# Kernel optimization log

Measured on AMD Instinct MI355X. Metric: run time of the kernel, lower is better.

The kernel has to match this reference:

```python
import jax, jax.numpy as jnp
import numpy as np

N = 10000      # atoms
F = 32         # nr_atom_basis
H = 7          # nr_heads
C = F * H      # nr_coefficients = 224
E = 200000     # edges
NRBF = 50
CUTOFF = 5.0
EPS = 1e-8


def _seg_sum(x, idx, n):
    return jax.ops.segment_sum(x, idx, num_segments=n)


def _seg_mean(x, idx, n):
    # torch scatter_reduce 'mean' with include_self=False: sum/count, 0 for empty segments
    s = _seg_sum(x, idx, n)
    cnt = _seg_sum(jnp.ones((x.shape[0],), x.dtype), idx, n)
    cnt = jnp.maximum(cnt, 1.0).reshape((n,) + (1,) * (x.ndim - 1))
    return s / cnt


def _scatter_softmax(w, idx, n):
    m = jax.ops.segment_max(w, idx, num_segments=n)
    m = jnp.where(jnp.isfinite(m), m, 0.0)  # guard empty segments
    e = jnp.exp(w - m[idx])
    s = _seg_sum(e, idx, n)
    return e / s[idx]


def setup_inputs():
    key = jax.random.key(0)
    ks = jax.random.split(key, 16)
    def w(k, shape, scale=0.1):
        return jax.random.normal(k, shape, jnp.float32) * scale
    return {
        "h": w(ks[0], (N, F), 1.0),
        "x": w(ks[1], (N, 3), 1.0),
        "v": w(ks[2], (N, 3), 0.1),
        "pairlist": jax.random.randint(ks[3], (2, E), 0, N),
        "w_in": w(ks[4], (2 * F, NRBF)), "b_in": jnp.zeros((NRBF,), jnp.float32),
        "w_e1": w(ks[5], (2 * F + NRBF + 1, F)), "b_e1": jnp.zeros((F,), jnp.float32),
        "w_e2": w(ks[6], (F, F)), "b_e2": jnp.zeros((F,), jnp.float32),
        "w_att": w(ks[7], (F, H)), "b_att": jnp.zeros((H,), jnp.float32),
        "w_n1": w(ks[8], (F + C + F, F)), "b_n1": jnp.zeros((F,), jnp.float32),
        "w_n2": w(ks[9], (F, F)), "b_n2": jnp.zeros((F,), jnp.float32),
        "w_pn1": w(ks[10], (C, F)), "b_pn1": jnp.zeros((F,), jnp.float32),
        "w_pn2": w(ks[11], (F, F)), "b_pn2": jnp.zeros((F,), jnp.float32),
        "w_v1": w(ks[12], (F, F)), "b_v1": jnp.zeros((F,), jnp.float32),
        "w_v2": w(ks[13], (F, 1)),
        "w_xmix": w(ks[14], (C, C)),
        "w_vmix": w(ks[15], (C, 1)),
    }


def reference(h, x, v, pairlist, w_in, b_in, w_e1, b_e1, w_e2, b_e2,
              w_att, b_att, w_n1, b_n1, w_n2, b_n2, w_pn1, b_pn1,
              w_pn2, b_pn2, w_v1, b_v1, w_v2, w_xmix, w_vmix):
    act = jax.nn.silu
    idx_i, idx_j = pairlist[0], pairlist[1]
    n = h.shape[0]

    r_ij = x[idx_j] - x[idx_i]                      # [E,3]
    d_ij = jnp.linalg.norm(r_ij, axis=-1)           # [E]
    dir_ij = r_ij / (d_ij[:, None] + EPS)           # [E,3]

    # edge model: continuous-filter conv with concatenation
    h_cat = jnp.concatenate([h[idx_i], h[idx_j]], axis=-1)           # [E,2F]
    centers = jnp.linspace(0.0, CUTOFF, NRBF)
    width = centers[1] - centers[0]
    rbf = jnp.exp(-0.5 * ((d_ij[:, None] - centers) / width) ** 2)   # [E,NRBF]
    filt = rbf * (h_cat @ w_in + b_in)                               # [E,NRBF]
    edge_in = jnp.concatenate([h_cat, filt, d_ij[:, None]], axis=-1)
    h_ij_edge = act(edge_in @ w_e1 + b_e1) @ w_e2 + b_e2             # [E,F]

    # semantic attention (scatter softmax over edges grouped by idx_i)
    att_w = jax.nn.celu(h_ij_edge @ w_att + b_att, alpha=2.0)        # [E,H]
    cut = 0.5 * (jnp.cos(jnp.pi * d_ij / CUTOFF) + 1.0) * (d_ij < CUTOFF)
    att = _scatter_softmax(att_w * cut[:, None], idx_i, n)           # [E,H]
    # einsum('pf,ph->pfh').reshape -> f-major, h-minor
    h_ij_sem = (h_ij_edge[:, :, None] * att[:, None, :]).reshape(-1, C)  # [E,C]
    h_i_sem = _seg_sum(h_ij_sem, idx_i, n)                           # [N,C]

    # equivariant combinations + spatial attention
    comb = jnp.tanh(h_ij_sem @ w_xmix)[:, :, None] * dir_ij[:, None, :]  # [E,C,3]
    comb_mean = _seg_mean(comb, idx_i, n)                            # [N,C,3]
    cnsq = jnp.sum(comb_mean ** 2, axis=-1)                          # [N,C]
    h_i_spatial = act(act(cnsq @ w_pn1 + b_pn1) @ w_pn2 + b_pn2)     # [N,F]

    # node update
    node_in = jnp.concatenate([h, h_i_sem, h_i_spatial], axis=-1)
    h_upd = h + act(act(node_in @ w_n1 + b_n1) @ w_n2 + b_n2)        # [N,F]

    # velocity update
    v_ij = jnp.einsum('ecx,c->ex', comb, w_vmix[:, 0])               # [E,3]
    dv = _seg_mean(v_ij, idx_i, n)                                   # [N,3]
    gate = 2.0 * jax.nn.sigmoid(act(h @ w_v1 + b_v1) @ w_v2)         # [N,1]
    v_upd = gate * v + dv
    x_upd = x + v_upd
    return h_upd, x_upd, v_upd
```

## Files before the change

kernel.cpp:

```cpp
#include <hip/hip_runtime.h>
#include <hip/hip_bf16.h>
#include <math.h>

typedef unsigned short u16;
typedef __attribute__((ext_vector_type(8))) short bf16x8;
typedef __attribute__((ext_vector_type(4))) float f32x4;

constexpr int kF    = 32;
constexpr int kH    = 7;
constexpr int kC    = 224;
constexpr int kRBF  = 50;
constexpr int kM    = 128;
constexpr int kStr  = 232;
constexpr int kUSt  = 36;
constexpr int kEM   = 128;
constexpr int kAStr = 136;
constexpr int kBStr = 40;
constexpr float kCut = 5.0f;
constexpr float kEps = 1e-8f;

__device__ __forceinline__ float silu_f(float a) { return a / (1.f + __expf(-a)); }
__device__ __forceinline__ float tanh_f(float x) {
    float e = __expf(2.f * x);
    return 1.f - 2.f / (e + 1.f);
}
__device__ __forceinline__ float bf2f(u16 u) {
    union { unsigned int i; float f; } v; v.i = ((unsigned int)u) << 16; return v.f;
}
__device__ __forceinline__ u16 f2bf(float f) {
    union { float f; unsigned int i; } v; v.f = f;
    unsigned int x = v.i;
    unsigned int round = ((x >> 16) & 1u) + 0x7fffu;
    return (u16)((x + round) >> 16);
}
__device__ __forceinline__ unsigned pk2(float a, float b) {
    union { __hip_bfloat162 h; unsigned u; } v;
    v.h = __float22bfloat162_rn(make_float2(a, b));
    return v.u;
}

__global__ __launch_bounds__(256) void init_kernel(
    const float* __restrict__ wx, const float* __restrict__ w_in,
    const float* __restrict__ w_e1, const float* __restrict__ w_e2,
    const float* __restrict__ w_att, const float* __restrict__ b_e2,
    const float* __restrict__ b_att, const float* __restrict__ w_n1,
    const int* __restrict__ pl,
    u16* __restrict__ wxT, u16* __restrict__ W1T, u16* __restrict__ W2T,
    u16* __restrict__ W3T, u16* __restrict__ W24T, u16* __restrict__ Wn1hT,
    float* __restrict__ b24, int* __restrict__ counts, int E_)
{
    int idx = blockIdx.x * 256 + threadIdx.x;
    if (idx < kC * kC) {
        int c = idx / kC, k = idx - c * kC;
        wxT[idx] = f2bf(wx[k * kC + c]);
    }
    for (int e = idx; e < E_; e += gridDim.x * 256) atomicAdd(&counts[pl[e]], 1);

    if (blockIdx.x == 0) {
        int t = threadIdx.x;
        for (int i = t; i < 64 * 64; i += 256) {
            int n = i >> 6, k = i & 63;
            W1T[i] = f2bf((n < kRBF) ? w_in[k * kRBF + n] : 0.f);
        }
        for (int i = t; i < 32 * 128; i += 256) {
            int n = i >> 7, k = i & 127;
            W2T[i] = f2bf((k < 115) ? w_e1[k * kF + n] : 0.f);
        }
        for (int i = t; i < 32 * 32; i += 256) {
            int n = i >> 5, k = i & 31;
            W3T[i] = f2bf(w_e2[k * kF + n]);
        }
        for (int i = t; i < 16 * 32; i += 256) {
            int n = i >> 5, k = i & 31;
            float a = 0.f;
            if (n < kH) for (int o = 0; o < kF; o++) a += w_e2[k * kF + o] * w_att[o * kH + n];
            W24T[i] = f2bf(a);
        }
        if (t < kH) {
            float a = b_att[t];
            for (int o = 0; o < kF; o++) a += b_e2[o] * w_att[o * kH + t];
            b24[t] = a;
        }
    }
    if (blockIdx.x == 1) {
        int t = threadIdx.x;
        for (int i = t; i < 32 * kC; i += 256) {
            int o = i / kC, k = i - o * kC;
            Wn1hT[i] = f2bf(w_n1[(kF + k) * kF + o]);
        }
    }
}

__global__ __launch_bounds__(1024) void scan_kernel(
    const int* __restrict__ counts, int* __restrict__ offsets, int n)
{
    __shared__ int buf[1024];
    int t = threadIdx.x;
    int chunk = (n + 1023) >> 10;
    int lo = t * chunk;
    int s = 0;
    for (int i = 0; i < chunk; i++) {
        int g = lo + i;
        if (g < n) s += counts[g];
    }
    buf[t] = s;
    __syncthreads();
    for (int off = 1; off < 1024; off <<= 1) {
        int v = (t >= off) ? buf[t - off] : 0;
        __syncthreads();
        buf[t] += v;
        __syncthreads();
    }
    int run = buf[t] - s;
    for (int i = 0; i < chunk; i++) {
        int g = lo + i;
        if (g < n) { offsets[g] = run; run += counts[g]; }
    }
    if (t == 1023) offsets[n] = buf[1023];
}

__global__ __launch_bounds__(256) void edge_kernel(
    const float* __restrict__ h, const float* __restrict__ x,
    const int* __restrict__ pl, const int* __restrict__ offs,
    int* __restrict__ cursor, int* __restrict__ nid, int E_,
    const float* __restrict__ b_in, const float* __restrict__ b_e1,
    const float* __restrict__ b_e2,
    const u16* __restrict__ W1T, const u16* __restrict__ W2T,
    const u16* __restrict__ W3T, const u16* __restrict__ W24T,
    const float* __restrict__ b24,
    u16* __restrict__ he_g, float* __restrict__ logit_g,
    float* __restrict__ dir_g)
{
    __shared__ __align__(16) u16 s_A[kEM][kAStr];
    __shared__ __align__(16) u16 s_t1[kEM][kBStr];
    __shared__ float s_d[kEM];
    __shared__ int   s_r[kEM];

    int t = threadIdx.x;
    int T0 = blockIdx.x * kEM;
    int w = t >> 6, lane = t & 63, quad = lane >> 4, l15 = lane & 15;

    {
        int e = t >> 1, half = t & 1;
        int ge = T0 + e;
        bool val = ge < E_;
        int i = 0, j = 0;
        if (val) { i = pl[ge]; j = pl[E_ + ge]; }
        const float4* pi = (const float4*)(h + (size_t)i * kF) + half * 4;
        const float4* pj = (const float4*)(h + (size_t)j * kF) + half * 4;
#pragma unroll
        for (int q = 0; q < 4; q++) {
            float4 a = val ? pi[q] : make_float4(0.f, 0.f, 0.f, 0.f);
            float4 b = val ? pj[q] : make_float4(0.f, 0.f, 0.f, 0.f);
            unsigned* di = (unsigned*)&s_A[e][half * 16 + 4 * q];
            di[0] = pk2(a.x, a.y); di[1] = pk2(a.z, a.w);
            unsigned* dj = (unsigned*)&s_A[e][kF + half * 16 + 4 * q];
            dj[0] = pk2(b.x, b.y); dj[1] = pk2(b.z, b.w);
        }
        if (half == 0) {
            float d = 0.f;
            int r = 0;
            if (val) {
                int p = atomicAdd(&cursor[i], 1);
                r = offs[i] + p;
                nid[r] = i;
                float r0 = x[j * 3 + 0] - x[i * 3 + 0];
                float r1 = x[j * 3 + 1] - x[i * 3 + 1];
                float r2 = x[j * 3 + 2] - x[i * 3 + 2];
                d = sqrtf(r0 * r0 + r1 * r1 + r2 * r2);
                float inv = 1.0f / (d + kEps);
                dir_g[(size_t)r * 3 + 0] = r0 * inv;
                dir_g[(size_t)r * 3 + 1] = r1 * inv;
                dir_g[(size_t)r * 3 + 2] = r2 * inv;
            }
            s_r[e] = r;
            s_d[e] = d;
            s_A[e][114] = f2bf(d);
            s_A[e][115] = 0;
            unsigned* z = (unsigned*)&s_A[e][116];
#pragma unroll
            for (int q = 0; q < 6; q++) z[q] = 0u;
        }
    }
    __syncthreads();

    const float invw = 49.0f / kCut;

    {
        bf16x8 a1[2][2];
#pragma unroll
        for (int rt = 0; rt < 2; rt++)
#pragma unroll
            for (int kt = 0; kt < 2; kt++)
                a1[rt][kt] = *(const bf16x8*)&s_A[32 * w + 16 * rt + l15][kt * 32 + quad * 8];
#pragma unroll
        for (int ct = 0; ct < 4; ct++) {
            int c = ct * 16 + l15;
            bf16x8 b0 = *(const bf16x8*)(W1T + (size_t)c * 64 + quad * 8);
            bf16x8 b1 = *(const bf16x8*)(W1T + (size_t)c * 64 + 32 + quad * 8);
            float bin = (c < kRBF) ? b_in[c] : 0.f;
#pragma unroll
            for (int rt = 0; rt < 2; rt++) {
                f32x4 acc = {0.f, 0.f, 0.f, 0.f};
                acc = __builtin_amdgcn_mfma_f32_16x16x32_bf16(a1[rt][0], b0, acc, 0, 0, 0);
                acc = __builtin_amdgcn_mfma_f32_16x16x32_bf16(a1[rt][1], b1, acc, 0, 0, 0);
                if (c < kRBF) {
#pragma unroll
                    for (int r = 0; r < 4; r++) {
                        int row = 32 * w + 16 * rt + quad * 4 + r;
                        float arg = s_d[row] * invw - (float)c;
                        float filt = __expf(-0.5f * arg * arg) * (acc[r] + bin);
                        s_A[row][64 + c] = f2bf(filt);
                    }
                }
            }
        }
    }

    {
        bf16x8 a2[2][4];
#pragma unroll
        for (int rt = 0; rt < 2; rt++)
#pragma unroll
            for (int kt = 0; kt < 4; kt++)
                a2[rt][kt] = *(const bf16x8*)&s_A[32 * w + 16 * rt + l15][kt * 32 + quad * 8];
#pragma unroll
        for (int ct = 0; ct < 2; ct++) {
            int c = ct * 16 + l15;
            bf16x8 bb[4];
#pragma unroll
            for (int kt = 0; kt < 4; kt++)
                bb[kt] = *(const bf16x8*)(W2T + (size_t)c * 128 + kt * 32 + quad * 8);
            float be = b_e1[c];
#pragma unroll
            for (int rt = 0; rt < 2; rt++) {
                f32x4 acc = {0.f, 0.f, 0.f, 0.f};
#pragma unroll
                for (int kt = 0; kt < 4; kt++)
                    acc = __builtin_amdgcn_mfma_f32_16x16x32_bf16(a2[rt][kt], bb[kt], acc, 0, 0, 0);
#pragma unroll
                for (int r = 0; r < 4; r++) {
                    int row = 32 * w + 16 * rt + quad * 4 + r;
                    s_t1[row][c] = f2bf(silu_f(acc[r] + be));
                }
            }
        }
    }

    {
        bf16x8 a3[2];
#pragma unroll
        for (int rt = 0; rt < 2; rt++)
            a3[rt] = *(const bf16x8*)&s_t1[32 * w + 16 * rt + l15][quad * 8];

#pragma unroll
        for (int ct = 0; ct < 2; ct++) {
            int c = ct * 16 + l15;
            bf16x8 b3 = *(const bf16x8*)(W3T + (size_t)c * 32 + quad * 8);
            float be = b_e2[c];
#pragma unroll
            for (int rt = 0; rt < 2; rt++) {
                f32x4 acc = {0.f, 0.f, 0.f, 0.f};
                acc = __builtin_amdgcn_mfma_f32_16x16x32_bf16(a3[rt], b3, acc, 0, 0, 0);
#pragma unroll
                for (int r = 0; r < 4; r++) {
                    int row = 32 * w + 16 * rt + quad * 4 + r;
                    int ge = T0 + row;
                    if (ge < E_) he_g[(size_t)s_r[row] * kF + c] = f2bf(acc[r] + be);
                }
            }
        }
        {
            bf16x8 b4 = *(const bf16x8*)(W24T + (size_t)l15 * 32 + quad * 8);
            float bb = (l15 < kH) ? b24[l15] : 0.f;
#pragma unroll
            for (int rt = 0; rt < 2; rt++) {
                f32x4 acc = {0.f, 0.f, 0.f, 0.f};
                acc = __builtin_amdgcn_mfma_f32_16x16x32_bf16(a3[rt], b4, acc, 0, 0, 0);
                if (l15 < kH) {
#pragma unroll
                    for (int r = 0; r < 4; r++) {
                        int row = 32 * w + 16 * rt + quad * 4 + r;
                        int ge = T0 + row;
                        if (ge < E_) {
                            float a = acc[r] + bb;
                            a = (a >= 0.f) ? a : 2.f * (__expf(0.5f * a) - 1.f);
                            float dd = s_d[row];
                            float cut = (dd < kCut)
                                ? 0.5f * (__cosf(0.62831853071795864f * dd) + 1.f) : 0.f;
                            logit_g[(size_t)s_r[row] * kH + l15] = a * cut;
                        }
                    }
                }
            }
        }
    }
}

__global__ __launch_bounds__(256) void stats_kernel(
    const float* __restrict__ logit_g, const int* __restrict__ offsets,
    float* __restrict__ m_g, float* __restrict__ invs_g, int N_)
{
    int grp  = threadIdx.x >> 5;
    int lane = threadIdx.x & 31;
    int node = blockIdx.x * 8 + grp;
    if (node >= N_) return;
    int base = offsets[node];
    int deg  = offsets[node + 1] - base;

    float m[kH], ss[kH];
#pragma unroll
    for (int hh = 0; hh < kH; hh++) { m[hh] = -1e30f; ss[hh] = 0.f; }
    for (int e = lane; e < deg; e += 32) {
        const float* lp = logit_g + (size_t)(base + e) * kH;
#pragma unroll
        for (int hh = 0; hh < kH; hh++) {
            float vv = lp[hh];
            if (vv > m[hh]) { ss[hh] *= __expf(m[hh] - vv); m[hh] = vv; }
            ss[hh] += __expf(vv - m[hh]);
        }
    }
#pragma unroll
    for (int hh = 0; hh < kH; hh++) {
        float mm = m[hh], s2 = ss[hh];
#pragma unroll
        for (int off = 16; off >= 1; off >>= 1) {
            float mo = __shfl_xor(mm, off);
            float so = __shfl_xor(s2, off);
            float mn = fmaxf(mm, mo);
            s2 = s2 * __expf(mm - mn) + so * __expf(mo - mn);
            mm = mn;
        }
        if (lane == 0) {
            m_g[(size_t)node * kH + hh] = mm;
            invs_g[(size_t)node * kH + hh] = (s2 > 0.f) ? 1.f / s2 : 0.f;
        }
    }
}

__global__ __launch_bounds__(256) void xmix_kernel(
    const u16* __restrict__ he_g, const float* __restrict__ logit_g,
    const float* __restrict__ dir_g, const int* __restrict__ nid,
    const float* __restrict__ m_g, const float* __restrict__ invs_g,
    const u16* __restrict__ wxT, const u16* __restrict__ Wn1hT, int E_,
    float* __restrict__ nodeacc, float* __restrict__ bpart, int* __restrict__ bid)
{
    __shared__ __align__(16) u16 s_buf[kM][kStr];
    __shared__ __align__(8)  u16 s_U[kM][kUSt];
    __shared__ float s_att[kM][kH];
    __shared__ __align__(16) float s_dir4[kM][4];
    __shared__ int   s_node[kM];
    __shared__ int   s_prev, s_next;

    int t = threadIdx.x;
    int T0 = blockIdx.x * kM;
    int cp = min(kM, E_ - T0);

    if (t < kM) s_node[t] = (T0 + t < E_) ? nid[T0 + t] : -1;
    if (t == 0) {
        s_prev = (T0 > 0) ? nid[T0 - 1] : -2;
        s_next = (T0 + cp < E_) ? nid[T0 + cp] : -2;
    }
    __syncthreads();

    int w    = t >> 6;
    int lane = t & 63;
    int quad = lane >> 4;
    int l15  = lane & 15;

    int ws = 32 * w;
    int we = min(ws + 32, cp);
    bool winvalid = (ws < cp);
    bool contL = false, contR = false;
    if (winvalid) {
        int nfirst = s_node[ws], nlast = s_node[we - 1];
        contL = (w == 0) ? (s_prev == nfirst) : (s_node[ws - 1] == nfirst);
        contR = (we == cp) ? (s_next == nlast) : (s_node[we] == nlast);
    }
    if (lane == 0) {
        int b0 = -1, b1 = -1;
        if (winvalid) {
            int nfirst = s_node[ws], nlast = s_node[we - 1];
            b0 = contL ? nfirst : -1;
            if (contR && !(nfirst == nlast && contL)) b1 = nlast;
        }
        bid[8 * blockIdx.x + 2 * w + 0] = b0;
        bid[8 * blockIdx.x + 2 * w + 1] = b1;
    }
    bool active_w = winvalid && (lane < 56);
    int c0 = 4 * lane;

    for (int idx = t; idx < kM * kH; idx += 256) {
        int e = idx / kH, hh = idx - e * kH;
        float a = 0.f;
        if (T0 + e < E_) {
            int nd = s_node[e];
            a = __expf(logit_g[(size_t)(T0 + e) * kH + hh] - m_g[(size_t)nd * kH + hh])
                * invs_g[(size_t)nd * kH + hh];
        }
        s_att[e][hh] = a;
    }
    for (int idx = t; idx < cp * 3; idx += 256) {
        int e = idx / 3, xx = idx - e * 3;
        s_dir4[e][xx] = dir_g[(size_t)(T0 + e) * 3 + xx];
    }
    __syncthreads();

#pragma unroll
    for (int p = 0; p < kM * kF / 256; p++) {
        int idx = t + 256 * p;
        int e = idx >> 5, f = idx & 31;
        float hv = (T0 + e < E_) ? bf2f(he_g[(size_t)(T0 + e) * kF + f]) : 0.f;
        float sv[7];
#pragma unroll
        for (int hh = 0; hh < kH; hh++) sv[hh] = hv * s_att[e][hh];
        u16* dst = &s_buf[e][f * 7];
        if ((f & 1) == 0) {
            *(unsigned*)(dst)     = pk2(sv[0], sv[1]);
            *(unsigned*)(dst + 2) = pk2(sv[2], sv[3]);
            *(unsigned*)(dst + 4) = pk2(sv[4], sv[5]);
            dst[6] = f2bf(sv[6]);
        } else {
            dst[0] = f2bf(sv[0]);
            *(unsigned*)(dst + 1) = pk2(sv[1], sv[2]);
            *(unsigned*)(dst + 3) = pk2(sv[3], sv[4]);
            *(unsigned*)(dst + 5) = pk2(sv[5], sv[6]);
        }
    }
    __syncthreads();

    bf16x8 afr[2][7];
#pragma unroll
    for (int rt = 0; rt < 2; rt++)
#pragma unroll
        for (int kt = 0; kt < 7; kt++)
            afr[rt][kt] = *(const bf16x8*)&s_buf[32 * w + 16 * rt + l15][kt * 32 + quad * 8];

    bf16x8 bb[3][7];
#pragma unroll
    for (int kt = 0; kt < 7; kt++)
        bb[0][kt] = *(const bf16x8*)(wxT + (size_t)l15 * kC + kt * 32 + quad * 8);
#pragma unroll
    for (int kt = 0; kt < 7; kt++)
        bb[1][kt] = *(const bf16x8*)(wxT + (size_t)(16 + l15) * kC + kt * 32 + quad * 8);

#pragma unroll
    for (int ct = 0; ct < 14; ct++) {
        const int cur = ct % 3;
        const int nxt = (ct + 2) % 3;
        if (ct < 12) {
            const u16* bp = wxT + (size_t)((ct + 2) * 16 + l15) * kC + quad * 8;
#pragma unroll
            for (int kt = 0; kt < 7; kt++) bb[nxt][kt] = *(const bf16x8*)(bp + kt * 32);
        }
        f32x4 acc0 = {0.f, 0.f, 0.f, 0.f};
        f32x4 acc1 = {0.f, 0.f, 0.f, 0.f};
#pragma unroll
        for (int kt = 0; kt < 7; kt++) {
            acc0 = __builtin_amdgcn_mfma_f32_16x16x32_bf16(afr[0][kt], bb[cur][kt], acc0, 0, 0, 0);
            acc1 = __builtin_amdgcn_mfma_f32_16x16x32_bf16(afr[1][kt], bb[cur][kt], acc1, 0, 0, 0);
        }
        int colg = ct * 16 + l15;
#pragma unroll
        for (int s = 0; s < 2; s++) {
            f32x4 ac = s ? acc1 : acc0;
            int rbase = 32 * w + 16 * s + quad * 4;
            unsigned p01 = pk2(tanh_f(ac[0]), tanh_f(ac[1]));
            unsigned p23 = pk2(tanh_f(ac[2]), tanh_f(ac[3]));
            s_buf[rbase + 0][colg] = (u16)p01;
            s_buf[rbase + 1][colg] = (u16)(p01 >> 16);
            s_buf[rbase + 2][colg] = (u16)p23;
            s_buf[rbase + 3][colg] = (u16)(p23 >> 16);
        }
    }

#pragma unroll
    for (int ut = 0; ut < 2; ut++) {
        bf16x8 ub[7];
        const u16* bp = Wn1hT + (size_t)(ut * 16 + l15) * kC + quad * 8;
#pragma unroll
        for (int kt = 0; kt < 7; kt++) ub[kt] = *(const bf16x8*)(bp + kt * 32);
        f32x4 acc0 = {0.f, 0.f, 0.f, 0.f};
        f32x4 acc1 = {0.f, 0.f, 0.f, 0.f};
#pragma unroll
        for (int kt = 0; kt < 7; kt++) {
            acc0 = __builtin_amdgcn_mfma_f32_16x16x32_bf16(afr[0][kt], ub[kt], acc0, 0, 0, 0);
            acc1 = __builtin_amdgcn_mfma_f32_16x16x32_bf16(afr[1][kt], ub[kt], acc1, 0, 0, 0);
        }
        int ucol = ut * 16 + l15;
#pragma unroll
        for (int s = 0; s < 2; s++) {
            f32x4 ac = s ? acc1 : acc0;
            int rbase = 32 * w + 16 * s + quad * 4;
#pragma unroll
            for (int r = 0; r < 4; r++) s_U[rbase + r][ucol] = f2bf(ac[r]);
        }
    }

    if (active_w) {
        bool uact = (lane < 8);
        float a0[4] = {0.f, 0.f, 0.f, 0.f};
        float a1[4] = {0.f, 0.f, 0.f, 0.f};
        float a2[4] = {0.f, 0.f, 0.f, 0.f};
        float uu[4] = {0.f, 0.f, 0.f, 0.f};
        int rs = ws;
        for (int e = ws; e < we; e++) {
            if (s_node[e] != s_node[rs]) {
                bool comp = (rs > ws) || !contL;
                float* p = comp ? (nodeacc + (size_t)s_node[rs] * 896)
                                : (bpart + (size_t)(8 * blockIdx.x + 2 * w) * 896);
                *(float4*)&p[c0]       = make_float4(a0[0], a0[1], a0[2], a0[3]);
                *(float4*)&p[224 + c0] = make_float4(a1[0], a1[1], a1[2], a1[3]);
                *(float4*)&p[448 + c0] = make_float4(a2[0], a2[1], a2[2], a2[3]);
                if (uact) *(float4*)&p[672 + c0] = make_float4(uu[0], uu[1], uu[2], uu[3]);
#pragma unroll
                for (int q = 0; q < 4; q++) { a0[q] = 0.f; a1[q] = 0.f; a2[q] = 0.f; uu[q] = 0.f; }
                rs = e;
            }
            float4 dd = *(const float4*)&s_dir4[e][0];
            uint2 pv = *(const uint2*)&s_buf[e][c0];
            float Tv[4];
            Tv[0] = bf2f((u16)pv.x); Tv[1] = bf2f((u16)(pv.x >> 16));
            Tv[2] = bf2f((u16)pv.y); Tv[3] = bf2f((u16)(pv.y >> 16));
#pragma unroll
            for (int q = 0; q < 4; q++) {
                a0[q] += Tv[q] * dd.x;
                a1[q] += Tv[q] * dd.y;
                a2[q] += Tv[q] * dd.z;
            }
            if (uact) {
                uint2 uv = *(const uint2*)&s_U[e][c0];
                uu[0] += bf2f((u16)uv.x); uu[1] += bf2f((u16)(uv.x >> 16));
                uu[2] += bf2f((u16)uv.y); uu[3] += bf2f((u16)(uv.y >> 16));
            }
        }
        bool t0 = (rs == ws);
        bool comp = ((!t0) || !contL) && !contR;
        float* p;
        if (comp) p = nodeacc + (size_t)s_node[rs] * 896;
        else {
            int slot = (t0 && contL) ? 0 : 1;
            p = bpart + (size_t)(8 * blockIdx.x + 2 * w + slot) * 896;
        }
        *(float4*)&p[c0]       = make_float4(a0[0], a0[1], a0[2], a0[3]);
        *(float4*)&p[224 + c0] = make_float4(a1[0], a1[1], a1[2], a1[3]);
        *(float4*)&p[448 + c0] = make_float4(a2[0], a2[1], a2[2], a2[3]);
        if (uact) *(float4*)&p[672 + c0] = make_float4(uu[0], uu[1], uu[2], uu[3]);
    }
}

__global__ __launch_bounds__(256) void node_kernel(
    const float* __restrict__ h, const float* __restrict__ x, const float* __restrict__ v,
    const float* __restrict__ nodeacc, const float* __restrict__ bpart,
    const int* __restrict__ bid, const int* __restrict__ offs,
    const float* __restrict__ w_n1, const float* __restrict__ b_n1,
    const float* __restrict__ w_n2, const float* __restrict__ b_n2,
    const float* __restrict__ w_pn1, const float* __restrict__ b_pn1,
    const float* __restrict__ w_pn2, const float* __restrict__ b_pn2,
    const float* __restrict__ w_v1, const float* __restrict__ b_v1,
    const float* __restrict__ w_v2, const float* __restrict__ w_vmix,
    float* __restrict__ out_h, float* __restrict__ out_x, float* __restrict__ out_v,
    int N_)
{
    __shared__ float s_cm[4][3][kC];
    __shared__ float s_cnsq[4][kC];
    __shared__ float s_ni[4][64];
    __shared__ float s_usum[4][kF];
    __shared__ float s_part[8][4][kF];
    __shared__ float s_hn[4][kF], s_sp1[4][kF], s_spat[4][kF], s_n1v[4][kF], s_g1[4][kF];
    __shared__ float s_pdv[4][3][8];
    __shared__ float s_gate[4], s_dv[4][3];

    int t = threadIdx.x;
    int n0 = blockIdx.x * 4;

    if (t < kC) {
        for (int nd = 0; nd < 4; nd++) {
            int node = n0 + nd;
            if (node >= N_) break;
            int base = offs[node], end = offs[node + 1];
            int deg = end - base;
            float a0 = 0.f, a1 = 0.f, a2 = 0.f, hh = 0.f;
            if (deg > 0) {
                int wlo = base >> 5, whi = (end - 1) >> 5;
                if (wlo == whi) {
                    const float* p = nodeacc + (size_t)node * 896;
                    a0 = p[t]; a1 = p[224 + t]; a2 = p[448 + t];
                    if (t < kF) hh = p[672 + t];
                } else {
                    for (int W = wlo; W <= whi; W++) {
#pragma unroll
                        for (int s = 0; s < 2; s++) {
                            if (bid[2 * W + s] == node) {
                                const float* p = bpart + (size_t)(2 * W + s) * 896;
                                a0 += p[t]; a1 += p[224 + t]; a2 += p[448 + t];
                                if (t < kF) hh += p[672 + t];
                            }
                        }
                    }
                }
            }
            float invc = 1.f / fmaxf((float)deg, 1.f);
            float m0 = a0 * invc, m1 = a1 * invc, m2 = a2 * invc;
            s_cm[nd][0][t] = m0; s_cm[nd][1][t] = m1; s_cm[nd][2][t] = m2;
            s_cnsq[nd][t] = m0 * m0 + m1 * m1 + m2 * m2;
            if (t < kF) s_usum[nd][t] = hh;
        }
    } else {
        int ln = t - 224;
        for (int nd = 0; nd < 4; nd++) {
            int node = n0 + nd;
            float hv = (node < N_) ? h[(size_t)node * kF + ln] : 0.f;
            s_hn[nd][ln] = hv;
            s_ni[nd][ln] = hv;
        }
    }
    __syncthreads();

    int o = t & 31, g = t >> 5;
    {
        float acc[4] = {0.f, 0.f, 0.f, 0.f};
        int cb = g * 28;
        for (int i = 0; i < 28; i++) {
            float wv = w_pn1[(cb + i) * kF + o];
#pragma unroll
            for (int nd = 0; nd < 4; nd++) acc[nd] += s_cnsq[nd][cb + i] * wv;
        }
#pragma unroll
        for (int nd = 0; nd < 4; nd++) s_part[g][nd][o] = acc[nd];
    }
    __syncthreads();
    if (t < 128) {
        int nd = t >> 5;
        float a = b_pn1[o];
#pragma unroll
        for (int g2 = 0; g2 < 8; g2++) a += s_part[g2][nd][o];
        s_sp1[nd][o] = silu_f(a);
    } else {
        int nd = (t - 128) >> 5;
        float a = b_v1[o];
        for (int f = 0; f < kF; f++) a += s_hn[nd][f] * w_v1[f * kF + o];
        s_g1[nd][o] = silu_f(a);
    }
    __syncthreads();
    if (t < 128) {
        int nd = t >> 5;
        float a = b_pn2[o];
        for (int o2 = 0; o2 < kF; o2++) a += s_sp1[nd][o2] * w_pn2[o2 * kF + o];
        s_spat[nd][o] = silu_f(a);
    } else if (t < 132) {
        int nd = t - 128;
        float a = 0.f;
        for (int o2 = 0; o2 < kF; o2++) a += s_g1[nd][o2] * w_v2[o2];
        s_gate[nd] = 2.f / (1.f + __expf(-a));
    } else if (t >= 160) {
        int q = t - 160; int nd = q / 24; int r = q - nd * 24;
        int xx = r >> 3, ln = r & 7;
        float a = 0.f;
        for (int c = ln; c < kC; c += 8) a += w_vmix[c] * s_cm[nd][xx][c];
        s_pdv[nd][xx][ln] = a;
    }
    __syncthreads();
    if (t < 128) {
        int nd = t >> 5;
        s_ni[nd][kF + o] = s_spat[nd][o];
    } else if (t < 140) {
        int q = t - 128; int nd = q / 3; int xx = q - nd * 3;
        float a = 0.f;
#pragma unroll
        for (int ln = 0; ln < 8; ln++) a += s_pdv[nd][xx][ln];
        s_dv[nd][xx] = a;
    }
    __syncthreads();
    {
        float acc[4] = {0.f, 0.f, 0.f, 0.f};
        int rb = g * 8;
        for (int i = 0; i < 8; i++) {
            int r = rb + i;
            int wr = (r < kF) ? r : (r + kC);
            float wv = w_n1[wr * kF + o];
#pragma unroll
            for (int nd = 0; nd < 4; nd++) acc[nd] += s_ni[nd][r] * wv;
        }
#pragma unroll
        for (int nd = 0; nd < 4; nd++) s_part[g][nd][o] = acc[nd];
    }
    __syncthreads();
    if (t < 128) {
        int nd = t >> 5;
        float a = b_n1[o] + s_usum[nd][o];
#pragma unroll
        for (int g2 = 0; g2 < 8; g2++) a += s_part[g2][nd][o];
        s_n1v[nd][o] = silu_f(a);
    }
    __syncthreads();
    if (t < 128) {
        int nd = t >> 5; int node = n0 + nd;
        if (node < N_) {
            float a = b_n2[o];
            for (int o2 = 0; o2 < kF; o2++) a += s_n1v[nd][o2] * w_n2[o2 * kF + o];
            out_h[(size_t)node * kF + o] = s_hn[nd][o] + silu_f(a);
        }
    } else if (t < 140) {
        int q = t - 128; int nd = q / 3; int xx = q - nd * 3;
        int node = n0 + nd;
        if (node < N_) {
            float vv = v[(size_t)node * 3 + xx];
            float vu = s_gate[nd] * vv + s_dv[nd][xx];
            out_v[(size_t)node * 3 + xx] = vu;
            out_x[(size_t)node * 3 + xx] = x[(size_t)node * 3 + xx] + vu;
        }
    }
}

extern "C" void kernel_launch(void* const* d_in, const int* in_sizes, int n_in,
                              void* d_out, int out_size, void* d_ws, size_t ws_size,
                              hipStream_t stream)
{
    const float* h      = (const float*)d_in[0];
    const float* x      = (const float*)d_in[1];
    const float* v      = (const float*)d_in[2];
    const int*   pl     = (const int*)d_in[3];
    const float* w_in   = (const float*)d_in[4];
    const float* b_in   = (const float*)d_in[5];
    const float* w_e1   = (const float*)d_in[6];
    const float* b_e1   = (const float*)d_in[7];
    const float* w_e2   = (const float*)d_in[8];
    const float* b_e2   = (const float*)d_in[9];
    const float* w_att  = (const float*)d_in[10];
    const float* b_att  = (const float*)d_in[11];
    const float* w_n1   = (const float*)d_in[12];
    const float* b_n1   = (const float*)d_in[13];
    const float* w_n2   = (const float*)d_in[14];
    const float* b_n2   = (const float*)d_in[15];
    const float* w_pn1  = (const float*)d_in[16];
    const float* b_pn1  = (const float*)d_in[17];
    const float* w_pn2  = (const float*)d_in[18];
    const float* b_pn2  = (const float*)d_in[19];
    const float* w_v1   = (const float*)d_in[20];
    const float* b_v1   = (const float*)d_in[21];
    const float* w_v2   = (const float*)d_in[22];
    const float* w_xmix = (const float*)d_in[23];
    const float* w_vmix = (const float*)d_in[24];

    const int E_ = in_sizes[3] / 2;
    const int N_ = in_sizes[0] / kF;
    const int nblk = (E_ + kM - 1) / kM;

    char* w = (char*)d_ws;
    u16*   wxT     = (u16*)w;   w += (size_t)kC * kC * 2;
    u16*   W1T     = (u16*)w;   w += (size_t)64 * 64 * 2;
    u16*   W2T     = (u16*)w;   w += (size_t)32 * 128 * 2;
    u16*   W3T     = (u16*)w;   w += (size_t)32 * 32 * 2;
    u16*   W24T    = (u16*)w;   w += (size_t)16 * 32 * 2;
    u16*   Wn1hT   = (u16*)w;   w += (size_t)32 * kC * 2;
    float* b24     = (float*)w; w += 8 * 4;
    u16*   he_g    = (u16*)w;   w += (size_t)E_ * kF * 2;
    float* logit_g = (float*)w; w += (size_t)E_ * kH * 4;
    float* dir_g   = (float*)w; w += (size_t)E_ * 3 * 4;
    float* m_g     = (float*)w; w += (size_t)N_ * kH * 4;
    float* invs_g  = (float*)w; w += (size_t)N_ * kH * 4;
    float* nodeacc = (float*)w; w += (size_t)N_ * 896 * 4;
    float* bpart   = (float*)w; w += (size_t)8 * nblk * 896 * 4;
    int*   bid     = (int*)w;   w += (size_t)8 * nblk * 4;
    int* counts    = (int*)w;   w += (size_t)N_ * 4;
    int* offs      = (int*)w;   w += (size_t)(N_ + 1) * 4;
    int* cursor    = (int*)w;   w += (size_t)N_ * 4;
    int* nid       = (int*)w;   w += (size_t)E_ * 4;

    float* out_h = (float*)d_out;
    float* out_x = out_h + (size_t)N_ * kF;
    float* out_v = out_x + (size_t)N_ * 3;

    hipMemsetAsync(counts, 0, (size_t)N_ * 4, stream);
    hipMemsetAsync(cursor, 0, (size_t)N_ * 4, stream);

    init_kernel<<<dim3((kC * kC + 255) / 256), dim3(256), 0, stream>>>(
        w_xmix, w_in, w_e1, w_e2, w_att, b_e2, b_att, w_n1, pl,
        wxT, W1T, W2T, W3T, W24T, Wn1hT, b24, counts, E_);

    scan_kernel<<<dim3(1), dim3(1024), 0, stream>>>(counts, offs, N_);

    edge_kernel<<<dim3((E_ + kEM - 1) / kEM), dim3(256), 0, stream>>>(
        h, x, pl, offs, cursor, nid, E_, b_in, b_e1, b_e2,
        W1T, W2T, W3T, W24T, b24, he_g, logit_g, dir_g);

    stats_kernel<<<dim3((N_ + 7) / 8), dim3(256), 0, stream>>>(
        logit_g, offs, m_g, invs_g, N_);

    xmix_kernel<<<dim3(nblk), dim3(256), 0, stream>>>(
        he_g, logit_g, dir_g, nid, m_g, invs_g, wxT, Wn1hT, E_,
        nodeacc, bpart, bid);

    node_kernel<<<dim3((N_ + 3) / 4), dim3(256), 0, stream>>>(
        h, x, v, nodeacc, bpart, bid, offs,
        w_n1, b_n1, w_n2, b_n2, w_pn1, b_pn1, w_pn2, b_pn2,
        w_v1, b_v1, w_v2, w_vmix, out_h, out_x, out_v, N_);
}
```

Measured before the change: 321.2 us.

## Compute normalized attention in stats kernel and prefetch edge features in xmix

The stats kernel now makes a second pass over each node's edges and writes the normalized softmax attention directly as bf16 per edge. The xmix kernel therefore no longer gathers per-node max and inverse-sum values or evaluates exp itself. Its loads of he, attention and direction are also issued before the first barrier, overlapping them with the node-id setup. This moves exp work and the scattered node gathers out of xmix, at the cost of an extra logit read and a bf16 write in stats, and rounds attention to bf16 before use.

Measured after the change: 319.2 us. Within noise of the previous version (-0.6%).

```diff
diff --git a/kernel.cpp b/kernel.cpp
--- a/kernel.cpp
+++ b/kernel.cpp
@@ -299,7 +299,7 @@
 
 __global__ __launch_bounds__(256) void stats_kernel(
     const float* __restrict__ logit_g, const int* __restrict__ offsets,
-    float* __restrict__ m_g, float* __restrict__ invs_g, int N_)
+    u16* __restrict__ att_g, int N_)
 {
     int grp  = threadIdx.x >> 5;
     int lane = threadIdx.x & 31;
@@ -331,17 +331,21 @@
             s2 = s2 * __expf(mm - mn) + so * __expf(mo - mn);
             mm = mn;
         }
-        if (lane == 0) {
-            m_g[(size_t)node * kH + hh] = mm;
-            invs_g[(size_t)node * kH + hh] = (s2 > 0.f) ? 1.f / s2 : 0.f;
-        }
+        m[hh] = mm;
+        ss[hh] = (s2 > 0.f) ? 1.f / s2 : 0.f;
+    }
+    for (int e = lane; e < deg; e += 32) {
+        const float* lp = logit_g + (size_t)(base + e) * kH;
+        u16* ap = att_g + (size_t)(base + e) * kH;
+#pragma unroll
+        for (int hh = 0; hh < kH; hh++)
+            ap[hh] = f2bf(__expf(lp[hh] - m[hh]) * ss[hh]);
     }
 }
 
 __global__ __launch_bounds__(256) void xmix_kernel(
-    const u16* __restrict__ he_g, const float* __restrict__ logit_g,
+    const u16* __restrict__ he_g, const u16* __restrict__ att_g,
     const float* __restrict__ dir_g, const int* __restrict__ nid,
-    const float* __restrict__ m_g, const float* __restrict__ invs_g,
     const u16* __restrict__ wxT, const u16* __restrict__ Wn1hT, int E_,
     float* __restrict__ nodeacc, float* __restrict__ bpart, int* __restrict__ bid)
 {
@@ -361,12 +365,29 @@
         s_prev = (T0 > 0) ? nid[T0 - 1] : -2;
         s_next = (T0 + cp < E_) ? nid[T0 + cp] : -2;
     }
-    __syncthreads();
 
     int w    = t >> 6;
     int lane = t & 63;
     int quad = lane >> 4;
     int l15  = lane & 15;
+
+    u16 hv16[16];
+#pragma unroll
+    for (int p = 0; p < 16; p++) {
+        int idx = t + 256 * p;
+        int e = idx >> 5, f = idx & 31;
+        hv16[p] = (T0 + e < E_) ? he_g[(size_t)(T0 + e) * kF + f] : (u16)0;
+    }
+
+    for (int idx = t; idx < kM * kH; idx += 256) {
+        int e = idx / kH;
+        s_att[e][idx - e * kH] = (T0 + e < E_) ? bf2f(att_g[(size_t)T0 * kH + idx]) : 0.f;
+    }
+    for (int idx = t; idx < cp * 3; idx += 256) {
+        int e = idx / 3, xx = idx - e * 3;
+        s_dir4[e][xx] = dir_g[(size_t)(T0 + e) * 3 + xx];
+    }
+    __syncthreads();
 
     int ws = 32 * w;
     int we = min(ws + 32, cp);
@@ -390,27 +411,11 @@
     bool active_w = winvalid && (lane < 56);
     int c0 = 4 * lane;
 
-    for (int idx = t; idx < kM * kH; idx += 256) {
-        int e = idx / kH, hh = idx - e * kH;
-        float a = 0.f;
-        if (T0 + e < E_) {
-            int nd = s_node[e];
-            a = __expf(logit_g[(size_t)(T0 + e) * kH + hh] - m_g[(size_t)nd * kH + hh])
-                * invs_g[(size_t)nd * kH + hh];
-        }
-        s_att[e][hh] = a;
-    }
-    for (int idx = t; idx < cp * 3; idx += 256) {
-        int e = idx / 3, xx = idx - e * 3;
-        s_dir4[e][xx] = dir_g[(size_t)(T0 + e) * 3 + xx];
-    }
-    __syncthreads();
-
-#pragma unroll
-    for (int p = 0; p < kM * kF / 256; p++) {
+#pragma unroll
+    for (int p = 0; p < 16; p++) {
         int idx = t + 256 * p;
         int e = idx >> 5, f = idx & 31;
-        float hv = (T0 + e < E_) ? bf2f(he_g[(size_t)(T0 + e) * kF + f]) : 0.f;
+        float hv = bf2f(hv16[p]);
         float sv[7];
 #pragma unroll
         for (int hh = 0; hh < kH; hh++) sv[hh] = hv * s_att[e][hh];
@@ -757,9 +762,8 @@
     float* b24     = (float*)w; w += 8 * 4;
     u16*   he_g    = (u16*)w;   w += (size_t)E_ * kF * 2;
     float* logit_g = (float*)w; w += (size_t)E_ * kH * 4;
+    u16*   att_g   = (u16*)w;   w += (size_t)E_ * kH * 2;
     float* dir_g   = (float*)w; w += (size_t)E_ * 3 * 4;
-    float* m_g     = (float*)w; w += (size_t)N_ * kH * 4;
-    float* invs_g  = (float*)w; w += (size_t)N_ * kH * 4;
     float* nodeacc = (float*)w; w += (size_t)N_ * 896 * 4;
     float* bpart   = (float*)w; w += (size_t)8 * nblk * 896 * 4;
     int*   bid     = (int*)w;   w += (size_t)8 * nblk * 4;
@@ -786,10 +790,10 @@
         W1T, W2T, W3T, W24T, b24, he_g, logit_g, dir_g);
 
     stats_kernel<<<dim3((N_ + 7) / 8), dim3(256), 0, stream>>>(
-        logit_g, offs, m_g, invs_g, N_);
+        logit_g, offs, att_g, N_);
 
     xmix_kernel<<<dim3(nblk), dim3(256), 0, stream>>>(
-        he_g, logit_g, dir_g, nid, m_g, invs_g, wxT, Wn1hT, E_,
+        he_g, att_g, dir_g, nid, wxT, Wn1hT, E_,
         nodeacc, bpart, bid);
 
     node_kernel<<<dim3((N_ + 3) / 4), dim3(256), 0, stream>>>(
```
